# Kernel tuning notes

Hardware: AMD Instinct MI355X
Metric: run time of the kernel (lower is better)

## Reference

```python
import jax, jax.numpy as jnp
import numpy as np

D = 1024
H = 16
DH = D // H  # 64


def setup_inputs() -> dict:
    key = jax.random.key(0)
    ks = jax.random.split(key, 7)
    X = jax.random.normal(ks[0], (2, 2048, D), dtype=jnp.float32)
    # Per-head projection weights stacked along head axis: [H, D, DH]
    s = 1.0 / np.sqrt(D)
    Wq = jax.random.uniform(ks[1], (H, D, DH), jnp.float32, -s, s)
    Wk = jax.random.uniform(ks[2], (H, D, DH), jnp.float32, -s, s)
    Wv = jax.random.uniform(ks[3], (H, D, DH), jnp.float32, -s, s)
    bq = jax.random.uniform(ks[4], (H, DH), jnp.float32, -s, s)
    bk = jax.random.uniform(ks[5], (H, DH), jnp.float32, -s, s)
    bv = jax.random.uniform(ks[6], (H, DH), jnp.float32, -s, s)
    return {"X": X, "Wq": Wq, "bq": bq, "Wk": Wk, "bk": bk, "Wv": Wv, "bv": bv}


def reference(X, Wq, bq, Wk, bk, Wv, bv):
    B, S, _ = X.shape
    # Per-head linear projections (batched over heads): [B, H, S, DH]
    Q = jnp.einsum('bsd,hde->bhse', X, Wq) + bq[None, :, None, :]
    K = jnp.einsum('bsd,hde->bhse', X, Wk) + bk[None, :, None, :]
    V = jnp.einsum('bsd,hde->bhse', X, Wv) + bv[None, :, None, :]
    scale = jnp.sqrt(jnp.asarray(DH, dtype=X.dtype))
    QK = jnp.einsum('bhse,bhte->bhst', Q, K) / scale  # [B, H, S, S]
    # Faithful to source: softmax over full row FIRST, then lower-tri mask
    # (post-softmax tril, no renormalization).
    sQK = jax.nn.softmax(QK, axis=-1)
    tril = jnp.tril(jnp.ones((S, S), dtype=X.dtype))
    sQK = sQK * tril
    out = jnp.einsum('bhst,bhte->bhse', sQK, V)  # [B, H, S, DH]
    # Concatenate heads along feature dim (torch.cat over per-head outputs)
    return out.transpose(0, 2, 1, 3).reshape(B, S, H * DH)
```

## Files before the change

### kernel.cpp

```cpp
#include <hip/hip_runtime.h>
#include <math.h>

#define B_  2
#define S_  2048
#define D_  1024
#define H_  16
#define DH_ 64

typedef unsigned short u16;
typedef unsigned int   u32;
typedef _Float16       f16;
typedef _Float16 half8  __attribute__((ext_vector_type(8)));
typedef _Float16 half4  __attribute__((ext_vector_type(4)));
typedef float    f32x4  __attribute__((ext_vector_type(4)));

#if __has_builtin(__builtin_amdgcn_exp2f)
#define EXP2(x) __builtin_amdgcn_exp2f(x)
#else
#define EXP2(x) exp2f(x)
#endif

__device__ __forceinline__ void st_u4(u16* p, uint4 v){
    u32* q = (u32*)p;
    q[0] = v.x; q[1] = v.y; q[2] = v.z; q[3] = v.w;
}
__device__ __forceinline__ u16 h_bits(f16 h){ return __builtin_bit_cast(u16, h); }

__global__ __launch_bounds__(256) void split_x_kernel(
    const float* __restrict__ X, u16* __restrict__ Xhi, u16* __restrict__ Xlo)
{
    const int idx = blockIdx.x * 256 + threadIdx.x;
    float4 v = ((const float4*)X)[idx];
    float fv[4] = {v.x, v.y, v.z, v.w};
    u16 hh[4], ll[4];
    #pragma unroll
    for (int j = 0; j < 4; ++j){
        f16 hi = (f16)fv[j];
        hh[j] = h_bits(hi);
        ll[j] = h_bits((f16)(fv[j] - (float)hi));
    }
    uint2 ph, pl;
    ph.x = hh[0] | ((u32)hh[1] << 16);
    ph.y = hh[2] | ((u32)hh[3] << 16);
    pl.x = ll[0] | ((u32)ll[1] << 16);
    pl.y = ll[2] | ((u32)ll[3] << 16);
    ((uint2*)Xhi)[idx] = ph;
    ((uint2*)Xlo)[idx] = pl;
}

__global__ __launch_bounds__(256) void convert_w_kernel(
    const float* __restrict__ Wq, const float* __restrict__ Wk,
    const float* __restrict__ Wv, u16* __restrict__ Wt)
{
    __shared__ float Wf[64][65];
    const int c  = threadIdx.x;
    const int d0 = blockIdx.x * 64;
    const int h  = blockIdx.y;
    const int which = blockIdx.z;
    const float* src = (which == 0) ? Wq : (which == 1) ? Wk : Wv;
    src += (size_t)h * D_ * DH_;

    #pragma unroll
    for (int it = 0; it < 4; ++it){
        int d  = (c >> 4) + 16 * it;
        int e4 = (c & 15) * 4;
        float4 v = *(const float4*)(src + (size_t)(d0 + d) * DH_ + e4);
        Wf[d][e4+0] = v.x; Wf[d][e4+1] = v.y; Wf[d][e4+2] = v.z; Wf[d][e4+3] = v.w;
    }
    __syncthreads();
    u16* dst = Wt + (size_t)(which * H_ + h) * DH_ * D_;
    #pragma unroll
    for (int it = 0; it < 4; ++it){
        int e  = (c >> 4) + 16 * it;
        int d4 = (c & 15) * 4;
        u16 q[4];
        #pragma unroll
        for (int j = 0; j < 4; ++j)
            q[j] = h_bits((f16)(Wf[d4 + j][e] * 64.0f));
        u32* p = (u32*)(dst + (size_t)e * D_ + d0 + d4);
        p[0] = q[0] | ((u32)q[1] << 16);
        p[1] = q[2] | ((u32)q[3] << 16);
    }
}

#define PKS 40

__global__ __launch_bounds__(256, 3) void proj_kernel(
    const u16* __restrict__ Xhi, const u16* __restrict__ Xlo,
    const u16* __restrict__ Wt,
    const float* __restrict__ bq, const float* __restrict__ bk,
    const float* __restrict__ bv,
    f16* __restrict__ Qh, f16* __restrict__ Kh, f16* __restrict__ Vh)
{
    __shared__ u16 XsHi[128 * PKS], XsLo[128 * PKS], Bs[128 * PKS];

    const int tid  = threadIdx.x;
    const int lane = tid & 63;
    const int w    = tid >> 6;
    const int quad = lane >> 4;
    const int ln   = lane & 15;
    const int wr   = (w >> 1) * 64;
    const int wc   = (w & 1) * 64;
    const int m0   = blockIdx.x * 128;
    const int c0   = blockIdx.y * 128;

    const int sr  = tid >> 2;
    const int sch = (tid & 3) * 8;

    const u16* xh0 = Xhi + (size_t)(m0 + sr) * D_ + sch;
    const u16* xh1 = xh0 + (size_t)64 * D_;
    const u16* xl0 = Xlo + (size_t)(m0 + sr) * D_ + sch;
    const u16* xl1 = xl0 + (size_t)64 * D_;
    const u16* wb0 = Wt  + (size_t)(c0 + sr) * D_ + sch;
    const u16* wb1 = wb0 + (size_t)64 * D_;

    uint4 rh0 = *(const uint4*)xh0, rh1 = *(const uint4*)xh1;
    uint4 rl0 = *(const uint4*)xl0, rl1 = *(const uint4*)xl1;
    uint4 rw0 = *(const uint4*)wb0, rw1 = *(const uint4*)wb1;

    f32x4 acc[4][4];
    #pragma unroll
    for (int i = 0; i < 4; ++i)
        #pragma unroll
        for (int j = 0; j < 4; ++j)
            acc[i][j] = (f32x4){0.f, 0.f, 0.f, 0.f};

    for (int k0 = 0; k0 < D_; k0 += 32){
        __syncthreads();
        *(uint4*)&XsHi[sr * PKS + sch]        = rh0;
        *(uint4*)&XsHi[(sr + 64) * PKS + sch] = rh1;
        *(uint4*)&XsLo[sr * PKS + sch]        = rl0;
        *(uint4*)&XsLo[(sr + 64) * PKS + sch] = rl1;
        *(uint4*)&Bs[sr * PKS + sch]          = rw0;
        *(uint4*)&Bs[(sr + 64) * PKS + sch]   = rw1;
        const int kn = k0 + 32;
        if (kn < D_){
            rh0 = *(const uint4*)(xh0 + kn); rh1 = *(const uint4*)(xh1 + kn);
            rl0 = *(const uint4*)(xl0 + kn); rl1 = *(const uint4*)(xl1 + kn);
            rw0 = *(const uint4*)(wb0 + kn); rw1 = *(const uint4*)(wb1 + kn);
        }
        __syncthreads();

        half8 ahi[4], alo[4], bf[4];
        #pragma unroll
        for (int mt = 0; mt < 4; ++mt){
            int row = wr + 16 * mt + ln;
            ahi[mt] = __builtin_bit_cast(half8, *(const uint4*)&XsHi[row * PKS + quad * 8]);
            alo[mt] = __builtin_bit_cast(half8, *(const uint4*)&XsLo[row * PKS + quad * 8]);
        }
        #pragma unroll
        for (int nt = 0; nt < 4; ++nt)
            bf[nt] = __builtin_bit_cast(half8,
                *(const uint4*)&Bs[(wc + 16 * nt + ln) * PKS + quad * 8]);
        #pragma unroll
        for (int mt = 0; mt < 4; ++mt)
            #pragma unroll
            for (int nt = 0; nt < 4; ++nt){
                acc[mt][nt] = __builtin_amdgcn_mfma_f32_16x16x32_f16(ahi[mt], bf[nt], acc[mt][nt], 0, 0, 0);
                acc[mt][nt] = __builtin_amdgcn_mfma_f32_16x16x32_f16(alo[mt], bf[nt], acc[mt][nt], 0, 0, 0);
            }
    }

    const float QSCALE = 0.125f * 1.44269504088896340736f;
    const float INV64  = 0.015625f;
    #pragma unroll
    for (int nt = 0; nt < 4; ++nt){
        int colg  = c0 + wc + 16 * nt + ln;
        int which = colg >> 10;
        int h     = (colg >> 6) & 15;
        int e     = colg & 63;
        const float* bp = (which == 0) ? bq : (which == 1) ? bk : bv;
        f16* op = (which == 0) ? Qh : (which == 1) ? Kh : Vh;
        float bias  = bp[h * DH_ + e];
        float scale = (which == 0) ? QSCALE : 1.0f;
        #pragma unroll
        for (int mt = 0; mt < 4; ++mt)
            #pragma unroll
            for (int r = 0; r < 4; ++r){
                int sg = m0 + wr + 16 * mt + 4 * quad + r;
                int b  = sg >> 11;
                int s  = sg & (S_ - 1);
                float val = (acc[mt][nt][r] * INV64 + bias) * scale;
                op[((size_t)(b * H_ + h) * S_ + s) * DH_ + e] = (f16)val;
            }
    }
}

__global__ __launch_bounds__(256) void transpose_v_kernel(
    const f16* __restrict__ Vh, f16* __restrict__ Vt)
{
    __shared__ u16 T[64 * 70];
    const int c  = threadIdx.x;
    const int t0 = blockIdx.x * 64;
    const int bh = blockIdx.y;
    const u16* src = (const u16*)Vh + (size_t)bh * S_ * DH_;
    #pragma unroll
    for (int it = 0; it < 2; ++it){
        int idx = c + 256 * it;
        int t  = idx >> 3;
        int ch = (idx & 7) * 8;
        st_u4(&T[t * 70 + ch], *(const uint4*)(src + (size_t)(t0 + t) * DH_ + ch));
    }
    __syncthreads();
    u16* dst = (u16*)Vt + (size_t)bh * DH_ * S_;
    #pragma unroll
    for (int it = 0; it < 2; ++it){
        int idx = c + 256 * it;
        int e  = idx >> 3;
        int tg = (idx & 7) * 8;
        u16 v[8];
        #pragma unroll
        for (int j = 0; j < 8; ++j) v[j] = T[(tg + j) * 70 + e];
        uint4 u;
        u.x = v[0] | ((u32)v[1] << 16);
        u.y = v[2] | ((u32)v[3] << 16);
        u.z = v[4] | ((u32)v[5] << 16);
        u.w = v[6] | ((u32)v[7] << 16);
        *(uint4*)(dst + (size_t)e * S_ + t0 + tg) = u;
    }
}

#define AKS 72

__global__ __launch_bounds__(256, 4) void attn_kernel(
    const f16* __restrict__ Qh, const f16* __restrict__ Kh,
    const f16* __restrict__ Vt, float* __restrict__ Out)
{
    __shared__ u16 Ks[64 * AKS];
    __shared__ u16 Vs[64 * AKS];

    const int tid  = threadIdx.x;
    const int lane = tid & 63;
    const int w    = tid >> 6;
    const int quad = lane >> 4;
    const int ln   = lane & 15;
    const int i    = blockIdx.x;
    const int h    = blockIdx.y;
    const int b    = blockIdx.z;
    const int bh   = b * H_ + h;
    const int sub  = w & 1;
    const int qbase = (w >> 1) ? (S_ - 32 * (i + 1) + 16 * sub)
                               : (32 * i + 16 * sub);
    const int vmax  = S_ - 32 * i - 1;

    const u16* Qg = (const u16*)Qh + (size_t)bh * S_ * DH_;
    const u16* Kg = (const u16*)Kh + (size_t)bh * S_ * DH_;
    const u16* Vg = (const u16*)Vt + (size_t)bh * DH_ * S_;

    half8 qf[2];
    #pragma unroll
    for (int ks = 0; ks < 2; ++ks)
        qf[ks] = __builtin_bit_cast(half8,
            *(const uint4*)(Qg + (size_t)(qbase + ln) * DH_ + 32 * ks + 8 * quad));

    const int kr = tid >> 3;
    const int kc = (tid & 7) * 8;

    uint4 kA = *(const uint4*)(Kg + (size_t)kr * DH_ + kc);
    uint4 kB = *(const uint4*)(Kg + (size_t)(kr + 32) * DH_ + kc);
    uint4 vA = *(const uint4*)(Vg + (size_t)kr * S_ + kc);
    uint4 vB = *(const uint4*)(Vg + (size_t)(kr + 32) * S_ + kc);

    float l_r = 0.f;
    f32x4 o_acc[4];
    #pragma unroll
    for (int nt = 0; nt < 4; ++nt) o_acc[nt] = (f32x4){0.f, 0.f, 0.f, 0.f};

    const int qrow   = qbase + ln;
    const int pv_lim = qbase + 15;

    for (int t0 = 0; t0 < S_; t0 += 64){
        __syncthreads();
        *(uint4*)&Ks[kr * AKS + kc]        = kA;
        *(uint4*)&Ks[(kr + 32) * AKS + kc] = kB;
        if (t0 <= vmax){
            *(uint4*)&Vs[kr * AKS + kc]        = vA;
            *(uint4*)&Vs[(kr + 32) * AKS + kc] = vB;
        }
        const int tn = t0 + 64;
        if (tn < S_){
            kA = *(const uint4*)(Kg + (size_t)(tn + kr) * DH_ + kc);
            kB = *(const uint4*)(Kg + (size_t)(tn + kr + 32) * DH_ + kc);
            if (tn <= vmax){
                vA = *(const uint4*)(Vg + (size_t)kr * S_ + tn + kc);
                vB = *(const uint4*)(Vg + (size_t)(kr + 32) * S_ + tn + kc);
            }
        }
        __syncthreads();

        f32x4 sc[4];
        #pragma unroll
        for (int mt = 0; mt < 4; ++mt) sc[mt] = (f32x4){0.f, 0.f, 0.f, 0.f};
        #pragma unroll
        for (int ks = 0; ks < 2; ++ks)
            #pragma unroll
            for (int mt = 0; mt < 4; ++mt){
                half8 kf = __builtin_bit_cast(half8,
                    *(const uint4*)&Ks[(16 * mt + ln) * AKS + 32 * ks + 8 * quad]);
                sc[mt] = __builtin_amdgcn_mfma_f32_16x16x32_f16(kf, qf[ks], sc[mt], 0, 0, 0);
            }

        #pragma unroll
        for (int mt = 0; mt < 4; ++mt)
            #pragma unroll
            for (int r = 0; r < 4; ++r)
                sc[mt][r] = EXP2(sc[mt][r]);
        float s = ((sc[0][0] + sc[0][1] + sc[0][2] + sc[0][3]) +
                   (sc[1][0] + sc[1][1] + sc[1][2] + sc[1][3])) +
                  ((sc[2][0] + sc[2][1] + sc[2][2] + sc[2][3]) +
                   (sc[3][0] + sc[3][1] + sc[3][2] + sc[3][3]));
        s += __shfl_xor(s, 16);
        s += __shfl_xor(s, 32);
        l_r += s;

        if (t0 <= pv_lim){
            half4 pf[4];
            #pragma unroll
            for (int mt = 0; mt < 4; ++mt){
                int tb = t0 + 16 * mt + 4 * quad;
                #pragma unroll
                for (int r = 0; r < 4; ++r)
                    pf[mt][r] = (tb + r > qrow) ? (f16)0.f : (f16)sc[mt][r];
            }
            #pragma unroll
            for (int nt = 0; nt < 4; ++nt)
                #pragma unroll
                for (int mt = 0; mt < 4; ++mt){
                    half4 vf = __builtin_bit_cast(half4,
                        *(const uint2*)&Vs[(16 * nt + ln) * AKS + 16 * mt + 4 * quad]);
                    o_acc[nt] = __builtin_amdgcn_mfma_f32_16x16x16f16(pf[mt], vf, o_acc[nt], 0, 0, 0);
                }
        }
    }

    #pragma unroll
    for (int r = 0; r < 4; ++r){
        float lv  = __shfl(l_r, (lane & 48) | (4 * quad + r));
        float inv = 1.0f / lv;
        int sg = qbase + 4 * quad + r;
        float* op = Out + ((size_t)b * S_ + sg) * D_ + h * DH_;
        #pragma unroll
        for (int nt = 0; nt < 4; ++nt)
            op[16 * nt + ln] = o_acc[nt][r] * inv;
    }
}

extern "C" void kernel_launch(void* const* d_in, const int* in_sizes, int n_in,
                              void* d_out, int out_size, void* d_ws, size_t ws_size,
                              hipStream_t stream)
{
    const float* X  = (const float*)d_in[0];
    const float* Wq = (const float*)d_in[1];
    const float* bq = (const float*)d_in[2];
    const float* Wk = (const float*)d_in[3];
    const float* bk = (const float*)d_in[4];
    const float* Wv = (const float*)d_in[5];
    const float* bv = (const float*)d_in[6];
    float* out = (float*)d_out;

    u16* Wt  = (u16*)d_ws;
    f16* Qh  = (f16*)(Wt + 3145728);
    f16* Kh  = Qh + 4194304;
    f16* Vh  = Kh + 4194304;
    u16* Xhi = (u16*)(Vh + 4194304);
    u16* Xlo = Xhi + 4194304;
    f16* Vt  = (f16*)Xhi;

    split_x_kernel<<<dim3(4096), 256, 0, stream>>>(X, Xhi, Xlo);
    convert_w_kernel<<<dim3(16, 16, 3), 256, 0, stream>>>(Wq, Wk, Wv, Wt);
    proj_kernel<<<dim3(32, 24), 256, 0, stream>>>(Xhi, Xlo, Wt, bq, bk, bv, Qh, Kh, Vh);
    transpose_v_kernel<<<dim3(32, 32), 256, 0, stream>>>(Vh, Vt);
    attn_kernel<<<dim3(32, 16, 2), 256, 0, stream>>>(Qh, Kh, Vt, out);
}
```

Baseline: 203.9 us.

## Merge prep kernels, write V transposed from projection, widen attention key tile

```diff
diff --git a/kernel.cpp b/kernel.cpp
--- a/kernel.cpp
+++ b/kernel.cpp
@@ -20,43 +20,43 @@
 #define EXP2(x) exp2f(x)
 #endif
 
-__device__ __forceinline__ void st_u4(u16* p, uint4 v){
-    u32* q = (u32*)p;
-    q[0] = v.x; q[1] = v.y; q[2] = v.z; q[3] = v.w;
-}
 __device__ __forceinline__ u16 h_bits(f16 h){ return __builtin_bit_cast(u16, h); }
 
-__global__ __launch_bounds__(256) void split_x_kernel(
-    const float* __restrict__ X, u16* __restrict__ Xhi, u16* __restrict__ Xlo)
-{
-    const int idx = blockIdx.x * 256 + threadIdx.x;
-    float4 v = ((const float4*)X)[idx];
-    float fv[4] = {v.x, v.y, v.z, v.w};
-    u16 hh[4], ll[4];
-    #pragma unroll
-    for (int j = 0; j < 4; ++j){
-        f16 hi = (f16)fv[j];
-        hh[j] = h_bits(hi);
-        ll[j] = h_bits((f16)(fv[j] - (float)hi));
-    }
-    uint2 ph, pl;
-    ph.x = hh[0] | ((u32)hh[1] << 16);
-    ph.y = hh[2] | ((u32)hh[3] << 16);
-    pl.x = ll[0] | ((u32)ll[1] << 16);
-    pl.y = ll[2] | ((u32)ll[3] << 16);
-    ((uint2*)Xhi)[idx] = ph;
-    ((uint2*)Xlo)[idx] = pl;
-}
-
-__global__ __launch_bounds__(256) void convert_w_kernel(
+__global__ __launch_bounds__(256) void prep_kernel(
+    const float* __restrict__ X,
     const float* __restrict__ Wq, const float* __restrict__ Wk,
-    const float* __restrict__ Wv, u16* __restrict__ Wt)
+    const float* __restrict__ Wv,
+    u16* __restrict__ Xhi, u16* __restrict__ Xlo, u16* __restrict__ Wt)
 {
     __shared__ float Wf[64][65];
-    const int c  = threadIdx.x;
-    const int d0 = blockIdx.x * 64;
-    const int h  = blockIdx.y;
-    const int which = blockIdx.z;
+    const int bid = blockIdx.x;
+    const int c   = threadIdx.x;
+
+    if (bid < 4096){
+        const int idx = bid * 256 + c;
+        float4 v = ((const float4*)X)[idx];
+        float fv[4] = {v.x, v.y, v.z, v.w};
+        u16 hh[4], ll[4];
+        #pragma unroll
+        for (int j = 0; j < 4; ++j){
+            f16 hi = (f16)fv[j];
+            hh[j] = h_bits(hi);
+            ll[j] = h_bits((f16)(fv[j] - (float)hi));
+        }
+        uint2 ph, pl;
+        ph.x = hh[0] | ((u32)hh[1] << 16);
+        ph.y = hh[2] | ((u32)hh[3] << 16);
+        pl.x = ll[0] | ((u32)ll[1] << 16);
+        pl.y = ll[2] | ((u32)ll[3] << 16);
+        ((uint2*)Xhi)[idx] = ph;
+        ((uint2*)Xlo)[idx] = pl;
+        return;
+    }
+
+    const int wb = bid - 4096;
+    const int d0 = (wb & 15) * 64;
+    const int h  = (wb >> 4) & 15;
+    const int which = wb >> 8;
     const float* src = (which == 0) ? Wq : (which == 1) ? Wk : Wv;
     src += (size_t)h * D_ * DH_;
 
@@ -90,7 +90,7 @@
     const u16* __restrict__ Wt,
     const float* __restrict__ bq, const float* __restrict__ bk,
     const float* __restrict__ bv,
-    f16* __restrict__ Qh, f16* __restrict__ Kh, f16* __restrict__ Vh)
+    f16* __restrict__ Qh, f16* __restrict__ Kh, f16* __restrict__ Vt)
 {
     __shared__ u16 XsHi[128 * PKS], XsLo[128 * PKS], Bs[128 * PKS];
 
@@ -170,64 +170,48 @@
         int h     = (colg >> 6) & 15;
         int e     = colg & 63;
         const float* bp = (which == 0) ? bq : (which == 1) ? bk : bv;
-        f16* op = (which == 0) ? Qh : (which == 1) ? Kh : Vh;
-        float bias  = bp[h * DH_ + e];
-        float scale = (which == 0) ? QSCALE : 1.0f;
-        #pragma unroll
-        for (int mt = 0; mt < 4; ++mt)
-            #pragma unroll
-            for (int r = 0; r < 4; ++r){
-                int sg = m0 + wr + 16 * mt + 4 * quad + r;
-                int b  = sg >> 11;
-                int s  = sg & (S_ - 1);
-                float val = (acc[mt][nt][r] * INV64 + bias) * scale;
-                op[((size_t)(b * H_ + h) * S_ + s) * DH_ + e] = (f16)val;
-            }
+        float bias = bp[h * DH_ + e];
+        if (which < 2){
+            f16* op = (which == 0) ? Qh : Kh;
+            float scale = (which == 0) ? QSCALE : 1.0f;
+            #pragma unroll
+            for (int mt = 0; mt < 4; ++mt)
+                #pragma unroll
+                for (int r = 0; r < 4; ++r){
+                    int sg = m0 + wr + 16 * mt + 4 * quad + r;
+                    int b  = sg >> 11;
+                    int s  = sg & (S_ - 1);
+                    float val = (acc[mt][nt][r] * INV64 + bias) * scale;
+                    op[((size_t)(b * H_ + h) * S_ + s) * DH_ + e] = (f16)val;
+                }
+        } else {
+            #pragma unroll
+            for (int mt = 0; mt < 4; ++mt){
+                int sg0 = m0 + wr + 16 * mt + 4 * quad;
+                int b   = sg0 >> 11;
+                int s0  = sg0 & (S_ - 1);
+                u16 p[4];
+                #pragma unroll
+                for (int r = 0; r < 4; ++r)
+                    p[r] = h_bits((f16)(acc[mt][nt][r] * INV64 + bias));
+                uint2 pk;
+                pk.x = p[0] | ((u32)p[1] << 16);
+                pk.y = p[2] | ((u32)p[3] << 16);
+                *(uint2*)((u16*)Vt + ((size_t)((b * H_ + h) * DH_ + e)) * S_ + s0) = pk;
+            }
+        }
     }
 }
 
-__global__ __launch_bounds__(256) void transpose_v_kernel(
-    const f16* __restrict__ Vh, f16* __restrict__ Vt)
-{
-    __shared__ u16 T[64 * 70];
-    const int c  = threadIdx.x;
-    const int t0 = blockIdx.x * 64;
-    const int bh = blockIdx.y;
-    const u16* src = (const u16*)Vh + (size_t)bh * S_ * DH_;
-    #pragma unroll
-    for (int it = 0; it < 2; ++it){
-        int idx = c + 256 * it;
-        int t  = idx >> 3;
-        int ch = (idx & 7) * 8;
-        st_u4(&T[t * 70 + ch], *(const uint4*)(src + (size_t)(t0 + t) * DH_ + ch));
-    }
-    __syncthreads();
-    u16* dst = (u16*)Vt + (size_t)bh * DH_ * S_;
-    #pragma unroll
-    for (int it = 0; it < 2; ++it){
-        int idx = c + 256 * it;
-        int e  = idx >> 3;
-        int tg = (idx & 7) * 8;
-        u16 v[8];
-        #pragma unroll
-        for (int j = 0; j < 8; ++j) v[j] = T[(tg + j) * 70 + e];
-        uint4 u;
-        u.x = v[0] | ((u32)v[1] << 16);
-        u.y = v[2] | ((u32)v[3] << 16);
-        u.z = v[4] | ((u32)v[5] << 16);
-        u.w = v[6] | ((u32)v[7] << 16);
-        *(uint4*)(dst + (size_t)e * S_ + t0 + tg) = u;
-    }
-}
-
 #define AKS 72
+#define VKS 136
 
 __global__ __launch_bounds__(256, 4) void attn_kernel(
     const f16* __restrict__ Qh, const f16* __restrict__ Kh,
     const f16* __restrict__ Vt, float* __restrict__ Out)
 {
-    __shared__ u16 Ks[64 * AKS];
-    __shared__ u16 Vs[64 * AKS];
+    __shared__ u16 Ks[128 * AKS];
+    __shared__ u16 Vs[64 * VKS];
 
     const int tid  = threadIdx.x;
     const int lane = tid & 63;
@@ -255,11 +239,15 @@
 
     const int kr = tid >> 3;
     const int kc = (tid & 7) * 8;
-
-    uint4 kA = *(const uint4*)(Kg + (size_t)kr * DH_ + kc);
-    uint4 kB = *(const uint4*)(Kg + (size_t)(kr + 32) * DH_ + kc);
-    uint4 vA = *(const uint4*)(Vg + (size_t)kr * S_ + kc);
-    uint4 vB = *(const uint4*)(Vg + (size_t)(kr + 32) * S_ + kc);
+    const int er = tid >> 2;
+    const int vj = (tid & 3) * 8;
+
+    uint4 kP[4], vP[4];
+    #pragma unroll
+    for (int j = 0; j < 4; ++j){
+        kP[j] = *(const uint4*)(Kg + (size_t)(kr + 32 * j) * DH_ + kc);
+        vP[j] = *(const uint4*)(Vg + (size_t)er * S_ + vj + 32 * j);
+    }
 
     float l_r = 0.f;
     f32x4 o_acc[4];
@@ -269,67 +257,69 @@
     const int qrow   = qbase + ln;
     const int pv_lim = qbase + 15;
 
-    for (int t0 = 0; t0 < S_; t0 += 64){
+    for (int t0 = 0; t0 < S_; t0 += 128){
         __syncthreads();
-        *(uint4*)&Ks[kr * AKS + kc]        = kA;
-        *(uint4*)&Ks[(kr + 32) * AKS + kc] = kB;
+        #pragma unroll
+        for (int j = 0; j < 4; ++j)
+            *(uint4*)&Ks[(kr + 32 * j) * AKS + kc] = kP[j];
         if (t0 <= vmax){
-            *(uint4*)&Vs[kr * AKS + kc]        = vA;
-            *(uint4*)&Vs[(kr + 32) * AKS + kc] = vB;
-        }
-        const int tn = t0 + 64;
+            #pragma unroll
+            for (int j = 0; j < 4; ++j)
+                *(uint4*)&Vs[er * VKS + vj + 32 * j] = vP[j];
+        }
+        const int tn = t0 + 128;
         if (tn < S_){
-            kA = *(const uint4*)(Kg + (size_t)(tn + kr) * DH_ + kc);
-            kB = *(const uint4*)(Kg + (size_t)(tn + kr + 32) * DH_ + kc);
+            #pragma unroll
+            for (int j = 0; j < 4; ++j)
+                kP[j] = *(const uint4*)(Kg + (size_t)(tn + kr + 32 * j) * DH_ + kc);
             if (tn <= vmax){
-                vA = *(const uint4*)(Vg + (size_t)kr * S_ + tn + kc);
-                vB = *(const uint4*)(Vg + (size_t)(kr + 32) * S_ + tn + kc);
+                #pragma unroll
+                for (int j = 0; j < 4; ++j)
+                    vP[j] = *(const uint4*)(Vg + (size_t)er * S_ + tn + vj + 32 * j);
             }
         }
         __syncthreads();
 
-        f32x4 sc[4];
-        #pragma unroll
-        for (int mt = 0; mt < 4; ++mt) sc[mt] = (f32x4){0.f, 0.f, 0.f, 0.f};
+        f32x4 sc[8];
+        #pragma unroll
+        for (int mt = 0; mt < 8; ++mt) sc[mt] = (f32x4){0.f, 0.f, 0.f, 0.f};
         #pragma unroll
         for (int ks = 0; ks < 2; ++ks)
             #pragma unroll
-            for (int mt = 0; mt < 4; ++mt){
+            for (int mt = 0; mt < 8; ++mt){
                 half8 kf = __builtin_bit_cast(half8,
                     *(const uint4*)&Ks[(16 * mt + ln) * AKS + 32 * ks + 8 * quad]);
                 sc[mt] = __builtin_amdgcn_mfma_f32_16x16x32_f16(kf, qf[ks], sc[mt], 0, 0, 0);
             }
 
         #pragma unroll
-        for (int mt = 0; mt < 4; ++mt)
+        for (int mt = 0; mt < 8; ++mt)
             #pragma unroll
             for (int r = 0; r < 4; ++r)
                 sc[mt][r] = EXP2(sc[mt][r]);
-        float s = ((sc[0][0] + sc[0][1] + sc[0][2] + sc[0][3]) +
-                   (sc[1][0] + sc[1][1] + sc[1][2] + sc[1][3])) +
-                  ((sc[2][0] + sc[2][1] + sc[2][2] + sc[2][3]) +
-                   (sc[3][0] + sc[3][1] + sc[3][2] + sc[3][3]));
+        float s = 0.f;
+        #pragma unroll
+        for (int mt = 0; mt < 8; ++mt)
+            s += (sc[mt][0] + sc[mt][1]) + (sc[mt][2] + sc[mt][3]);
         s += __shfl_xor(s, 16);
         s += __shfl_xor(s, 32);
         l_r += s;
 
-        if (t0 <= pv_lim){
-            half4 pf[4];
-            #pragma unroll
-            for (int mt = 0; mt < 4; ++mt){
+        #pragma unroll
+        for (int mt = 0; mt < 8; ++mt){
+            if (t0 + 16 * mt <= pv_lim){
                 int tb = t0 + 16 * mt + 4 * quad;
+                half4 pf;
                 #pragma unroll
                 for (int r = 0; r < 4; ++r)
-                    pf[mt][r] = (tb + r > qrow) ? (f16)0.f : (f16)sc[mt][r];
-            }
-            #pragma unroll
-            for (int nt = 0; nt < 4; ++nt)
-                #pragma unroll
-                for (int mt = 0; mt < 4; ++mt){
+                    pf[r] = (tb + r > qrow) ? (f16)0.f : (f16)sc[mt][r];
+                #pragma unroll
+                for (int nt = 0; nt < 4; ++nt){
                     half4 vf = __builtin_bit_cast(half4,
-                        *(const uint2*)&Vs[(16 * nt + ln) * AKS + 16 * mt + 4 * quad]);
-                    o_acc[nt] = __builtin_amdgcn_mfma_f32_16x16x16f16(pf[mt], vf, o_acc[nt], 0, 0, 0);
+                        *(const uint2*)&Vs[(16 * nt + ln) * VKS + 16 * mt + 4 * quad]);
+                    o_acc[nt] = __builtin_amdgcn_mfma_f32_16x16x16f16(pf, vf, o_acc[nt], 0, 0, 0);
                 }
+            }
         }
     }
 
@@ -361,14 +351,11 @@
     u16* Wt  = (u16*)d_ws;
     f16* Qh  = (f16*)(Wt + 3145728);
     f16* Kh  = Qh + 4194304;
-    f16* Vh  = Kh + 4194304;
-    u16* Xhi = (u16*)(Vh + 4194304);
+    f16* Vt  = Kh + 4194304;
+    u16* Xhi = (u16*)(Vt + 4194304);
     u16* Xlo = Xhi + 4194304;
-    f16* Vt  = (f16*)Xhi;
-
-    split_x_kernel<<<dim3(4096), 256, 0, stream>>>(X, Xhi, Xlo);
-    convert_w_kernel<<<dim3(16, 16, 3), 256, 0, stream>>>(Wq, Wk, Wv, Wt);
-    proj_kernel<<<dim3(32, 24), 256, 0, stream>>>(Xhi, Xlo, Wt, bq, bk, bv, Qh, Kh, Vh);
-    transpose_v_kernel<<<dim3(32, 32), 256, 0, stream>>>(Vh, Vt);
+
+    prep_kernel<<<dim3(4096 + 768), 256, 0, stream>>>(X, Wq, Wk, Wv, Xhi, Xlo, Wt);
+    proj_kernel<<<dim3(32, 24), 256, 0, stream>>>(Xhi, Xlo, Wt, bq, bk, bv, Qh, Kh, Vt);
     attn_kernel<<<dim3(32, 16, 2), 256, 0, stream>>>(Qh, Kh, Vt, out);
 }
```

Result: slower. 299.7 us (+47.0%).
